# Optimization experiments

Measured on AMD Instinct MI355X. Metric: run time of the kernel, lower is better.

## Reference

```python
import jax, jax.numpy as jnp
import numpy as np

N_SRC, N_DST, N_EDGE, D = 100000, 40000, 600000, 128
LN_EPS = 1e-5

def _mlp(x, w1, b1, w2, b2, g, beta):
    # anemoi MLP: Linear -> SiLU -> Linear -> LayerNorm
    h = jax.nn.silu(x @ w1 + b1)
    h = h @ w2 + b2
    mu = jnp.mean(h, axis=-1, keepdims=True)
    var = jnp.var(h, axis=-1, keepdims=True)
    return (h - mu) * jax.lax.rsqrt(var + LN_EPS) * g + beta

def setup_inputs() -> dict:
    key = jax.random.key(0)
    ks = jax.random.split(key, 12)
    def rn(k, shape, scale):
        return jax.random.normal(k, shape, dtype=jnp.float32) * scale
    w_scale = 0.05
    return dict(
        x_src=rn(ks[0], (N_SRC, D), 1.0),
        x_dst=rn(ks[1], (N_DST, D), 1.0),
        edge_attr=rn(ks[2], (N_EDGE, D), 1.0),
        edge_index=jnp.stack([
            jax.random.randint(ks[3], (N_EDGE,), 0, N_SRC),
            jax.random.randint(ks[4], (N_EDGE,), 0, N_DST)]).astype(jnp.int32),
        edge_w1=rn(ks[5], (3 * D, D), w_scale), edge_b1=jnp.zeros((D,), jnp.float32),
        edge_w2=rn(ks[6], (D, D), w_scale), edge_b2=jnp.zeros((D,), jnp.float32),
        edge_g=jnp.ones((D,), jnp.float32), edge_beta=jnp.zeros((D,), jnp.float32),
        node_w1=rn(ks[7], (2 * D, D), w_scale), node_b1=jnp.zeros((D,), jnp.float32),
        node_w2=rn(ks[8], (D, D), w_scale), node_b2=jnp.zeros((D,), jnp.float32),
        node_g=jnp.ones((D,), jnp.float32), node_beta=jnp.zeros((D,), jnp.float32),
    )

def reference(x_src, x_dst, edge_attr, edge_index,
              edge_w1, edge_b1, edge_w2, edge_b2, edge_g, edge_beta,
              node_w1, node_b1, node_w2, node_b2, node_g, node_beta):
    src, dst = edge_index[0], edge_index[1]
    # GraphConv message: x_i = dst node feats, x_j = src node feats (PyG source_to_target)
    x_i = x_dst[dst]              # [E, D] gather
    x_j = x_src[src]              # [E, D] gather
    edges_new = _mlp(jnp.concatenate([x_i, x_j, edge_attr], axis=-1),
                     edge_w1, edge_b1, edge_w2, edge_b2, edge_g, edge_beta) + edge_attr
    # sum-aggregate messages to dst nodes (chunked sum == single sum)
    agg = jax.ops.segment_sum(edges_new, dst, num_segments=N_DST)  # [N_DST, D]
    nodes_new_dst = _mlp(jnp.concatenate([x_dst, agg], axis=-1),
                         node_w1, node_b1, node_w2, node_b2, node_g, node_beta) + x_dst
    # update_src_nodes=True branch
    nodes_new_src = _mlp(jnp.concatenate([x_src, x_src], axis=-1),
                         node_w1, node_b1, node_w2, node_b2, node_g, node_beta) + x_src
    return nodes_new_src, nodes_new_dst, edges_new
```

## Files before the change

kernel.cpp:

```cpp
#include <hip/hip_runtime.h>
#include <hip/hip_bf16.h>

#define NSRC  100000
#define NDST  40000
#define NEDGE 600000

#define GB_OFF     0ull
#define W1F_OFF    2048ull
#define W2F_OFF    (W1F_OFF + 98304ull)
#define NW1F_OFF   (W2F_OFF + 32768ull)
#define NW2F_OFF   (NW1F_OFF + 65536ull)
#define NW1SF_OFF  (NW2F_OFF + 32768ull)
#define DEG_OFF    (NW1SF_OFF + 32768ull)
#define CSR_OFF    (DEG_OFF + 160000ull)
#define CUR_OFF    (CSR_OFF + 160016ull)
#define CE_OFF     (CUR_OFF + 160000ull)
#define BSUM_OFF   (CE_OFF + 2400000ull)
#define WS_REQUIRED (BSUM_OFF + 1024ull)

typedef __bf16 bf16;
typedef __attribute__((ext_vector_type(8))) __bf16 bf16x8;
typedef __attribute__((ext_vector_type(4))) float f32x4;

__device__ __forceinline__ unsigned short bfbits(float f) {
    return __builtin_bit_cast(unsigned short, (__bf16)f);
}

__device__ __forceinline__ f32x4 mfma16(bf16x8 a, bf16x8 b, f32x4 c) {
    return __builtin_amdgcn_mfma_f32_16x16x32_bf16(a, b, c, 0, 0, 0);
}

__device__ __forceinline__ bf16x8 pack8(float4 a, float4 b) {
    union { uint4 u; bf16x8 v; } o;
    o.u.x = (unsigned)bfbits(a.x) | ((unsigned)bfbits(a.y) << 16);
    o.u.y = (unsigned)bfbits(a.z) | ((unsigned)bfbits(a.w) << 16);
    o.u.z = (unsigned)bfbits(b.x) | ((unsigned)bfbits(b.y) << 16);
    o.u.w = (unsigned)bfbits(b.z) | ((unsigned)bfbits(b.w) << 16);
    return o.v;
}

__device__ __forceinline__ bf16x8 cvt8p(const float* p) {
    return pack8(*(const float4*)p, *(const float4*)(p + 4));
}

__device__ __forceinline__ void cvt8hl_v(float4 a, float4 b, bf16x8& hi, bf16x8& lo) {
    float v[8] = {a.x, a.y, a.z, a.w, b.x, b.y, b.z, b.w};
    union { uint4 u; bf16x8 v; } H, L;
    unsigned hw[8], lw[8];
#pragma unroll
    for (int i = 0; i < 8; ++i) {
        bf16 h = (bf16)v[i];
        hw[i] = (unsigned)__builtin_bit_cast(unsigned short, h);
        lw[i] = (unsigned)bfbits(v[i] - (float)h);
    }
    H.u.x = hw[0] | (hw[1] << 16); H.u.y = hw[2] | (hw[3] << 16);
    H.u.z = hw[4] | (hw[5] << 16); H.u.w = hw[6] | (hw[7] << 16);
    L.u.x = lw[0] | (lw[1] << 16); L.u.y = lw[2] | (lw[3] << 16);
    L.u.z = lw[4] | (lw[5] << 16); L.u.w = lw[6] | (lw[7] << 16);
    hi = H.v; lo = L.v;
}

__global__ __launch_bounds__(256) void prep_kernel(
    const float* __restrict__ w1, const float* __restrict__ w2,
    const float* __restrict__ nw1, const float* __restrict__ nw2,
    bf16* __restrict__ w1f, bf16* __restrict__ w2f,
    bf16* __restrict__ nw1f, bf16* __restrict__ nw2f, bf16* __restrict__ nw1sf) {
    int i = blockIdx.x * 256 + threadIdx.x;
    if (i < 49152) {
        int j = i & 7, lane = (i >> 3) & 63, f = (i >> 9) & 3;
        int rest = i >> 11; int ks = rest % 12, wc = rest / 12;
        int k = ks * 32 + (lane >> 4) * 8 + j;
        int n = wc * 64 + f * 16 + (lane & 15);
        w1f[i] = (bf16)w1[k * 128 + n];
    } else if (i < 65536) {
        int q = i - 49152;
        int j = q & 7, lane = (q >> 3) & 63, f = (q >> 9) & 3;
        int rest = q >> 11; int ks = rest & 3, wc = rest >> 2;
        int k = ks * 32 + (lane >> 4) * 8 + j;
        int n = wc * 64 + f * 16 + (lane & 15);
        w2f[q] = (bf16)w2[k * 128 + n];
    } else if (i < 98304) {
        int q = i - 65536;
        int j = q & 7, lane = (q >> 3) & 63, f = (q >> 9) & 3;
        int rest = q >> 11; int ks = rest & 7, wc = rest >> 3;
        int k = ks * 32 + (lane >> 4) * 8 + j;
        int n = wc * 64 + f * 16 + (lane & 15);
        nw1f[q] = (bf16)nw1[k * 128 + n];
    } else if (i < 114688) {
        int q = i - 98304;
        int j = q & 7, lane = (q >> 3) & 63, f = (q >> 9) & 3;
        int rest = q >> 11; int ks = rest & 3, wc = rest >> 2;
        int k = ks * 32 + (lane >> 4) * 8 + j;
        int n = wc * 64 + f * 16 + (lane & 15);
        nw2f[q] = (bf16)nw2[k * 128 + n];
    } else {
        int q = i - 114688;
        int j = q & 7, lane = (q >> 3) & 63, f = (q >> 9) & 3;
        int rest = q >> 11; int ks = rest & 3, wc = rest >> 2;
        int k = ks * 32 + (lane >> 4) * 8 + j;
        int n = wc * 64 + f * 16 + (lane & 15);
        nw1sf[q] = (bf16)(nw1[k * 128 + n] + nw1[(k + 128) * 128 + n]);
    }
}

__global__ void select_gbeta(const float* __restrict__ a, const float* __restrict__ b,
                             float* __restrict__ g_out, float* __restrict__ beta_out) {
    int t = threadIdx.x;
    bool a_is_g = (a[0] == 1.0f);
    const float* g  = a_is_g ? a : b;
    const float* be = a_is_g ? b : a;
    g_out[t]    = g[t];
    beta_out[t] = be[t];
}

__global__ __launch_bounds__(256) void hist_kernel(const int* __restrict__ eidx,
                                                   int* __restrict__ deg) {
    int e = blockIdx.x * 256 + threadIdx.x;
    if (e < NEDGE) {
        int d = min(max(eidx[NEDGE + e], 0), NDST - 1);
        atomicAdd(&deg[d], 1);
    }
}

__global__ __launch_bounds__(256) void scan1_kernel(const int* __restrict__ deg,
                                                    int* __restrict__ bsum) {
    __shared__ int wsum[4];
    int i = blockIdx.x * 256 + threadIdx.x;
    int v = (i < NDST) ? deg[i] : 0;
#pragma unroll
    for (int m = 1; m < 64; m <<= 1) v += __shfl_xor(v, m, 64);
    if ((threadIdx.x & 63) == 0) wsum[threadIdx.x >> 6] = v;
    __syncthreads();
    if (threadIdx.x == 0) bsum[blockIdx.x] = wsum[0] + wsum[1] + wsum[2] + wsum[3];
}

__global__ __launch_bounds__(256) void scan2_kernel(int* __restrict__ bsum, int nb) {
    __shared__ int buf[256];
    int t = threadIdx.x;
    int v = (t < nb) ? bsum[t] : 0;
    buf[t] = v;
    __syncthreads();
    for (int off = 1; off < 256; off <<= 1) {
        int add = (t >= off) ? buf[t - off] : 0;
        __syncthreads();
        buf[t] += add;
        __syncthreads();
    }
    if (t < nb) bsum[t] = buf[t] - v;
}

__global__ __launch_bounds__(256) void scan3_kernel(const int* __restrict__ deg,
                                                    const int* __restrict__ bsum,
                                                    int* __restrict__ csr,
                                                    int* __restrict__ cur) {
    __shared__ int buf[256];
    int i = blockIdx.x * 256 + threadIdx.x;
    int t = threadIdx.x;
    int v = (i < NDST) ? deg[i] : 0;
    buf[t] = v;
    __syncthreads();
    for (int off = 1; off < 256; off <<= 1) {
        int add = (t >= off) ? buf[t - off] : 0;
        __syncthreads();
        buf[t] += add;
        __syncthreads();
    }
    if (i < NDST) {
        int excl = bsum[blockIdx.x] + buf[t] - v;
        csr[i] = excl;
        cur[i] = excl;
        if (i == NDST - 1) csr[NDST] = NEDGE;
    }
}

__global__ __launch_bounds__(256) void scatter_kernel(const int* __restrict__ eidx,
                                                      int* __restrict__ cur,
                                                      int* __restrict__ ce) {
    int e = blockIdx.x * 256 + threadIdx.x;
    if (e < NEDGE) {
        int d = min(max(eidx[NEDGE + e], 0), NDST - 1);
        int pos = atomicAdd(&cur[d], 1);
        ce[pos] = e;
    }
}

__device__ __forceinline__ void mlp_tail(
    f32x4 (&acc)[2][4], char* sH, float* redS, float* redQ,
    const bf16x8* w2v, const float* b1, const float* b2,
    const float* g, const float* be,
    int wr, int wc, int lr, int lg, int lane,
    float (&outv)[2][4][4])
{
    {
        float b1c[4];
#pragma unroll
        for (int fc = 0; fc < 4; ++fc) b1c[fc] = b1[wc * 64 + fc * 16 + lr];
#pragma unroll
        for (int fr = 0; fr < 2; ++fr)
#pragma unroll
            for (int fc = 0; fc < 4; ++fc)
#pragma unroll
                for (int rg = 0; rg < 4; ++rg) {
                    int row = wr * 32 + fr * 16 + lg * 4 + rg;
                    int col = wc * 64 + fc * 16 + lr;
                    float v = acc[fr][fc][rg] + b1c[fc];
                    v = v / (1.f + __expf(-v));
                    *(bf16*)(sH + ((row * 256 + col * 2) ^ ((row & 7) << 4))) = (bf16)v;
                }
    }
    __syncthreads();

#pragma unroll
    for (int i = 0; i < 2; ++i)
#pragma unroll
        for (int j = 0; j < 4; ++j) acc[i][j] = f32x4{0.f, 0.f, 0.f, 0.f};
#pragma unroll
    for (int ks = 0; ks < 4; ++ks) {
        bf16x8 a[2], b[4];
#pragma unroll
        for (int f = 0; f < 2; ++f) {
            int ra = wr * 32 + f * 16 + lr;
            a[f] = *(const bf16x8*)(sH + ((ra * 256 + ks * 64 + lg * 16) ^ ((ra & 7) << 4)));
        }
#pragma unroll
        for (int fc = 0; fc < 4; ++fc)
            b[fc] = w2v[((wc * 4 + ks) * 4 + fc) * 64 + lane];
#pragma unroll
        for (int i = 0; i < 2; ++i)
#pragma unroll
            for (int j = 0; j < 4; ++j)
                acc[i][j] = mfma16(a[i], b[j], acc[i][j]);
    }

    float b2c[4], gc[4], bc[4];
#pragma unroll
    for (int fc = 0; fc < 4; ++fc) {
        int col = wc * 64 + fc * 16 + lr;
        b2c[fc] = b2[col]; gc[fc] = g[col]; bc[fc] = be[col];
    }
#pragma unroll
    for (int fr = 0; fr < 2; ++fr)
#pragma unroll
        for (int rg = 0; rg < 4; ++rg) {
            float s = 0.f, sq = 0.f;
#pragma unroll
            for (int fc = 0; fc < 4; ++fc) {
                float v = acc[fr][fc][rg] + b2c[fc];
                acc[fr][fc][rg] = v;
                s += v; sq += v * v;
            }
#pragma unroll
            for (int m = 1; m < 16; m <<= 1) {
                s  += __shfl_xor(s, m, 64);
                sq += __shfl_xor(sq, m, 64);
            }
            if (lr == 0) {
                int row = wr * 32 + fr * 16 + lg * 4 + rg;
                redS[row * 2 + wc] = s;
                redQ[row * 2 + wc] = sq;
            }
        }
    __syncthreads();

#pragma unroll
    for (int fr = 0; fr < 2; ++fr)
#pragma unroll
        for (int rg = 0; rg < 4; ++rg) {
            int row = wr * 32 + fr * 16 + lg * 4 + rg;
            float s  = redS[row * 2] + redS[row * 2 + 1];
            float sq = redQ[row * 2] + redQ[row * 2 + 1];
            float mean = s * (1.f / 128.f);
            float var  = fmaxf(sq * (1.f / 128.f) - mean * mean, 0.f);
            float rstd = rsqrtf(var + 1e-5f);
#pragma unroll
            for (int fc = 0; fc < 4; ++fc)
                outv[fr][fc][rg] = (acc[fr][fc][rg] - mean) * rstd * gc[fc] + bc[fc];
        }
}

__global__ __launch_bounds__(256, 3) void edge_mfma(
    const float* __restrict__ xsrc, const float* __restrict__ xdst,
    const float* __restrict__ attr, const int* __restrict__ eidx,
    const bf16* __restrict__ w1f,  const bf16* __restrict__ w2f,
    const float* __restrict__ b1,  const float* __restrict__ b2,
    const float* __restrict__ g,   const float* __restrict__ be,
    float* __restrict__ oute)
{
    __shared__ __align__(16) char sH[32768];
    __shared__ float redS[256], redQ[256];
    __shared__ int sS[128], sD[128];

    const int t = threadIdx.x;
    const long e0 = (long)blockIdx.x * 128;
    if (t < 128) {
        long e = e0 + t; if (e >= NEDGE) e = NEDGE - 1;
        sS[t] = min(max(eidx[e], 0), NSRC - 1);
        sD[t] = min(max(eidx[NEDGE + e], 0), NDST - 1);
    }
    __syncthreads();

    const int lane = t & 63, w = t >> 6;
    const int wr = w >> 1, wc = w & 1;
    const int lr = lane & 15, lg = lane >> 4;

    const float* xi[4]; const float* xj[4]; const float* at[4];
#pragma unroll
    for (int f = 0; f < 4; ++f) {
        int row = wr * 64 + f * 16 + lr;
        long e = e0 + row; if (e >= NEDGE) e = NEDGE - 1;
        xi[f] = xdst + (long)sD[row] * 128;
        xj[f] = xsrc + (long)sS[row] * 128;
        at[f] = attr + e * 128;
    }

    const bf16x8* w1v = (const bf16x8*)w1f;
    const bf16x8* w2v = (const bf16x8*)w2f;

    f32x4 acc[4][4];
#pragma unroll
    for (int i = 0; i < 4; ++i)
#pragma unroll
        for (int j = 0; j < 4; ++j) acc[i][j] = f32x4{0.f, 0.f, 0.f, 0.f};

#pragma unroll
    for (int ks = 0; ks < 12; ++ks) {
        int koff = (ks & 3) * 32 + lg * 8;
        bf16x8 a[4], b[4];
#pragma unroll
        for (int f = 0; f < 4; ++f) {
            const float* p = (ks < 4 ? xi[f] : ks < 8 ? xj[f] : at[f]) + koff;
            a[f] = cvt8p(p);
        }
#pragma unroll
        for (int fc = 0; fc < 4; ++fc)
            b[fc] = w1v[((wc * 12 + ks) * 4 + fc) * 64 + lane];
#pragma unroll
        for (int f = 0; f < 4; ++f)
#pragma unroll
            for (int j = 0; j < 4; ++j)
                acc[f][j] = mfma16(a[f], b[j], acc[f][j]);
    }

    {
        float b1c[4];
#pragma unroll
        for (int fc = 0; fc < 4; ++fc) b1c[fc] = b1[wc * 64 + fc * 16 + lr];
#pragma unroll
        for (int fr = 0; fr < 4; ++fr)
#pragma unroll
            for (int fc = 0; fc < 4; ++fc)
#pragma unroll
                for (int rg = 0; rg < 4; ++rg) {
                    int row = wr * 64 + fr * 16 + lg * 4 + rg;
                    int col = wc * 64 + fc * 16 + lr;
                    float v = acc[fr][fc][rg] + b1c[fc];
                    v = v / (1.f + __expf(-v));
                    *(bf16*)(sH + ((row * 256 + col * 2) ^ ((row & 7) << 4))) = (bf16)v;
                }
    }
    __syncthreads();

#pragma unroll
    for (int i = 0; i < 4; ++i)
#pragma unroll
        for (int j = 0; j < 4; ++j) acc[i][j] = f32x4{0.f, 0.f, 0.f, 0.f};
#pragma unroll
    for (int ks = 0; ks < 4; ++ks) {
        bf16x8 a[4], b[4];
#pragma unroll
        for (int f = 0; f < 4; ++f) {
            int ra = wr * 64 + f * 16 + lr;
            a[f] = *(const bf16x8*)(sH + ((ra * 256 + ks * 64 + lg * 16) ^ ((ra & 7) << 4)));
        }
#pragma unroll
        for (int fc = 0; fc < 4; ++fc)
            b[fc] = w2v[((wc * 4 + ks) * 4 + fc) * 64 + lane];
#pragma unroll
        for (int f = 0; f < 4; ++f)
#pragma unroll
            for (int j = 0; j < 4; ++j)
                acc[f][j] = mfma16(a[f], b[j], acc[f][j]);
    }

    float b2c[4], gc[4], bc[4];
#pragma unroll
    for (int fc = 0; fc < 4; ++fc) {
        int col = wc * 64 + fc * 16 + lr;
        b2c[fc] = b2[col]; gc[fc] = g[col]; bc[fc] = be[col];
    }
#pragma unroll
    for (int fr = 0; fr < 4; ++fr)
#pragma unroll
        for (int rg = 0; rg < 4; ++rg) {
            float s = 0.f, sq = 0.f;
#pragma unroll
            for (int fc = 0; fc < 4; ++fc) {
                float v = acc[fr][fc][rg] + b2c[fc];
                acc[fr][fc][rg] = v;
                s += v; sq += v * v;
            }
#pragma unroll
            for (int m = 1; m < 16; m <<= 1) {
                s  += __shfl_xor(s, m, 64);
                sq += __shfl_xor(sq, m, 64);
            }
            if (lr == 0) {
                int row = wr * 64 + fr * 16 + lg * 4 + rg;
                redS[row * 2 + wc] = s;
                redQ[row * 2 + wc] = sq;
            }
        }
    __syncthreads();

#pragma unroll
    for (int fr = 0; fr < 4; ++fr)
#pragma unroll
        for (int rg = 0; rg < 4; ++rg) {
            int row = wr * 64 + fr * 16 + lg * 4 + rg;
            float s  = redS[row * 2] + redS[row * 2 + 1];
            float sq = redQ[row * 2] + redQ[row * 2 + 1];
            float mean = s * (1.f / 128.f);
            float var  = fmaxf(sq * (1.f / 128.f) - mean * mean, 0.f);
            float rstd = rsqrtf(var + 1e-5f);
            long e = e0 + row;
            if (e < NEDGE) {
#pragma unroll
                for (int fc = 0; fc < 4; ++fc) {
                    int col = wc * 64 + fc * 16 + lr;
                    float v = (acc[fr][fc][rg] - mean) * rstd * gc[fc] + bc[fc];
                    oute[e * 128 + col] = v + attr[e * 128 + col];
                }
            }
        }
}

__global__ __launch_bounds__(256, 4) void node_src_mfma(
    const float* __restrict__ xsrc,
    const bf16* __restrict__ nw1sf, const bf16* __restrict__ nw2f,
    const float* __restrict__ b1, const float* __restrict__ b2,
    const float* __restrict__ g,  const float* __restrict__ be,
    float* __restrict__ outp)
{
    __shared__ __align__(16) char sH[16384];
    __shared__ float redS[128], redQ[128];

    const int t = threadIdx.x;
    const long r0 = (long)blockIdx.x * 64;
    const int lane = t & 63, w = t >> 6;
    const int wr = w >> 1, wc = w & 1;
    const int lr = lane & 15, lg = lane >> 4;

    long gr0 = r0 + wr * 32 + lr;      if (gr0 >= NSRC) gr0 = NSRC - 1;
    long gr1 = r0 + wr * 32 + 16 + lr; if (gr1 >= NSRC) gr1 = NSRC - 1;
    const float* x0 = xsrc + gr0 * 128;
    const float* x1 = xsrc + gr1 * 128;

    const bf16x8* w1v = (const bf16x8*)nw1sf;
    const bf16x8* w2v = (const bf16x8*)nw2f;

    f32x4 acc[2][4];
#pragma unroll
    for (int i = 0; i < 2; ++i)
#pragma unroll
        for (int j = 0; j < 4; ++j) acc[i][j] = f32x4{0.f, 0.f, 0.f, 0.f};

#pragma unroll
    for (int ks = 0; ks < 4; ++ks) {
        int k0 = ks * 32 + lg * 8;
        bf16x8 a0 = cvt8p(x0 + k0);
        bf16x8 a1 = cvt8p(x1 + k0);
        bf16x8 b[4];
#pragma unroll
        for (int fc = 0; fc < 4; ++fc)
            b[fc] = w1v[((wc * 4 + ks) * 4 + fc) * 64 + lane];
#pragma unroll
        for (int j = 0; j < 4; ++j) {
            acc[0][j] = mfma16(a0, b[j], acc[0][j]);
            acc[1][j] = mfma16(a1, b[j], acc[1][j]);
        }
    }

    float outv[2][4][4];
    mlp_tail(acc, sH, redS, redQ, w2v, b1, b2, g, be, wr, wc, lr, lg, lane, outv);

#pragma unroll
    for (int fr = 0; fr < 2; ++fr)
#pragma unroll
        for (int rg = 0; rg < 4; ++rg) {
            int row = wr * 32 + fr * 16 + lg * 4 + rg;
            long gr = r0 + row;
            if (gr < NSRC) {
#pragma unroll
                for (int fc = 0; fc < 4; ++fc) {
                    int col = wc * 64 + fc * 16 + lr;
                    outp[gr * 128 + col] = outv[fr][fc][rg] + xsrc[gr * 128 + col];
                }
            }
        }
}

__global__ __launch_bounds__(256, 3) void node_dst_mfma(
    const float* __restrict__ xdst, const float* __restrict__ oute,
    const int* __restrict__ csr, const int* __restrict__ ce,
    const bf16* __restrict__ nw1f, const bf16* __restrict__ nw2f,
    const float* __restrict__ b1, const float* __restrict__ b2,
    const float* __restrict__ g,  const float* __restrict__ be,
    float* __restrict__ outp)
{
    __shared__ __align__(16) char sAgg[32768];
    __shared__ __align__(16) char sH[16384];
    __shared__ float redS[128], redQ[128];

    const int t = threadIdx.x;
    const long r0 = (long)blockIdx.x * 64;
    const int lane = t & 63, w = t >> 6;
    const int wr = w >> 1, wc = w & 1;
    const int lr = lane & 15, lg = lane >> 4;

    for (int rr = 0; rr < 16; ++rr) {
        int row = w * 16 + rr;
        long gr = r0 + row;
        int s0 = csr[gr], s1 = csr[gr + 1];
        float ax = 0.f, ay = 0.f, az = 0.f, aw2 = 0.f;
        for (int i = s0 + (lane >> 5); i < s1; i += 2) {
            int e = ce[i];
            float4 vv = *(const float4*)(oute + (long)e * 128 + (lane & 31) * 4);
            ax += vv.x; ay += vv.y; az += vv.z; aw2 += vv.w;
        }
        ax  += __shfl_xor(ax, 32);
        ay  += __shfl_xor(ay, 32);
        az  += __shfl_xor(az, 32);
        aw2 += __shfl_xor(aw2, 32);
        if (lane < 32) {
            float4 o; o.x = ax; o.y = ay; o.z = az; o.w = aw2;
            *(float4*)(sAgg + ((row * 512 + (lane & 31) * 16) ^ ((row & 7) << 4))) = o;
        }
    }
    __syncthreads();

    long gr0 = r0 + wr * 32 + lr;
    long gr1 = gr0 + 16;
    const float* x0 = xdst + gr0 * 128;
    const float* x1 = xdst + gr1 * 128;

    const bf16x8* w1v = (const bf16x8*)nw1f;
    const bf16x8* w2v = (const bf16x8*)nw2f;

    f32x4 acc[2][4];
#pragma unroll
    for (int i = 0; i < 2; ++i)
#pragma unroll
        for (int j = 0; j < 4; ++j) acc[i][j] = f32x4{0.f, 0.f, 0.f, 0.f};

#pragma unroll
    for (int ks = 0; ks < 4; ++ks) {
        int k0 = ks * 32 + lg * 8;
        bf16x8 a0 = cvt8p(x0 + k0);
        bf16x8 a1 = cvt8p(x1 + k0);
        bf16x8 b[4];
#pragma unroll
        for (int fc = 0; fc < 4; ++fc)
            b[fc] = w1v[((wc * 8 + ks) * 4 + fc) * 64 + lane];
#pragma unroll
        for (int j = 0; j < 4; ++j) {
            acc[0][j] = mfma16(a0, b[j], acc[0][j]);
            acc[1][j] = mfma16(a1, b[j], acc[1][j]);
        }
    }
    const int rowl0 = wr * 32 + lr, rowl1 = rowl0 + 16;
#pragma unroll
    for (int ks = 0; ks < 4; ++ks) {
        int base0 = rowl0 * 512 + ks * 128 + lg * 32;
        int base1 = rowl1 * 512 + ks * 128 + lg * 32;
        float4 aA = *(const float4*)(sAgg + ((base0)      ^ ((rowl0 & 7) << 4)));
        float4 aB = *(const float4*)(sAgg + ((base0 + 16) ^ ((rowl0 & 7) << 4)));
        float4 bA = *(const float4*)(sAgg + ((base1)      ^ ((rowl1 & 7) << 4)));
        float4 bB = *(const float4*)(sAgg + ((base1 + 16) ^ ((rowl1 & 7) << 4)));
        bf16x8 h0, l0, h1, l1;
        cvt8hl_v(aA, aB, h0, l0);
        cvt8hl_v(bA, bB, h1, l1);
        bf16x8 b[4];
#pragma unroll
        for (int fc = 0; fc < 4; ++fc)
            b[fc] = w1v[((wc * 8 + 4 + ks) * 4 + fc) * 64 + lane];
#pragma unroll
        for (int j = 0; j < 4; ++j) {
            acc[0][j] = mfma16(h0, b[j], acc[0][j]);
            acc[1][j] = mfma16(h1, b[j], acc[1][j]);
            acc[0][j] = mfma16(l0, b[j], acc[0][j]);
            acc[1][j] = mfma16(l1, b[j], acc[1][j]);
        }
    }

    float outv[2][4][4];
    mlp_tail(acc, sH, redS, redQ, w2v, b1, b2, g, be, wr, wc, lr, lg, lane, outv);

#pragma unroll
    for (int fr = 0; fr < 2; ++fr)
#pragma unroll
        for (int rg = 0; rg < 4; ++rg) {
            int row = wr * 32 + fr * 16 + lg * 4 + rg;
            long gr = r0 + row;
#pragma unroll
            for (int fc = 0; fc < 4; ++fc) {
                int col = wc * 64 + fc * 16 + lr;
                outp[gr * 128 + col] = outv[fr][fc][rg] + xdst[gr * 128 + col];
            }
        }
}

extern "C" void kernel_launch(void* const* d_in, const int* in_sizes, int n_in,
                              void* d_out, int out_size, void* d_ws, size_t ws_size,
                              hipStream_t stream) {
    if (ws_size < WS_REQUIRED) return;

    const float* xsrc = nullptr; const float* xdst = nullptr;
    const float* attr = nullptr; const int*   eidx = nullptr;
    const float* ew1  = nullptr; const float* nw1  = nullptr;
    const float* w2s[2] = {nullptr, nullptr}; int n16384 = 0;
    const float* v128[8] = {nullptr}; int n128 = 0;

    for (int i = 0; i < n_in; ++i) {
        switch (in_sizes[i]) {
            case 12800000: xsrc = (const float*)d_in[i]; break;
            case 5120000:  xdst = (const float*)d_in[i]; break;
            case 76800000: attr = (const float*)d_in[i]; break;
            case 1200000:  eidx = (const int*)d_in[i];   break;
            case 49152:    ew1  = (const float*)d_in[i]; break;
            case 32768:    nw1  = (const float*)d_in[i]; break;
            case 16384:    if (n16384 < 2) w2s[n16384++] = (const float*)d_in[i]; break;
            case 128:      if (n128 < 8)   v128[n128++]  = (const float*)d_in[i]; break;
            default: break;
        }
    }
    if (!xsrc || !xdst || !attr || !eidx || !ew1 || !nw1 || n16384 != 2 || n128 != 8)
        return;

    const float* ew2 = w2s[0];
    const float* nw2 = w2s[1];
    const float* eb1 = v128[0]; const float* eb2 = v128[1];
    const float* egA = v128[2]; const float* egB = v128[3];
    const float* nb1 = v128[4]; const float* nb2 = v128[5];
    const float* ngA = v128[6]; const float* ngB = v128[7];

    char* ws = (char*)d_ws;
    float* egv  = (float*)(ws + GB_OFF);
    float* ebv  = egv + 128;
    float* ngv  = ebv + 128;
    float* nbv  = ngv + 128;
    bf16* w1f   = (bf16*)(ws + W1F_OFF);
    bf16* w2f   = (bf16*)(ws + W2F_OFF);
    bf16* nw1f  = (bf16*)(ws + NW1F_OFF);
    bf16* nw2f  = (bf16*)(ws + NW2F_OFF);
    bf16* nw1sf = (bf16*)(ws + NW1SF_OFF);
    int*  deg   = (int*)(ws + DEG_OFF);
    int*  csr   = (int*)(ws + CSR_OFF);
    int*  cur   = (int*)(ws + CUR_OFF);
    int*  ce    = (int*)(ws + CE_OFF);
    int*  bsum  = (int*)(ws + BSUM_OFF);

    float* out      = (float*)d_out;
    float* out_src  = out;
    float* out_dst  = out + (long)NSRC * 128;
    float* out_edge = out + (long)(NSRC + NDST) * 128;

    const int NB = (NDST + 255) / 256;

    hipMemsetAsync(deg, 0, (size_t)NDST * sizeof(int), stream);
    select_gbeta<<<1, 128, 0, stream>>>(egA, egB, egv, ebv);
    select_gbeta<<<1, 128, 0, stream>>>(ngA, ngB, ngv, nbv);
    prep_kernel<<<512, 256, 0, stream>>>(ew1, ew2, nw1, nw2, w1f, w2f, nw1f, nw2f, nw1sf);

    hist_kernel<<<(NEDGE + 255) / 256, 256, 0, stream>>>(eidx, deg);
    scan1_kernel<<<NB, 256, 0, stream>>>(deg, bsum);
    scan2_kernel<<<1, 256, 0, stream>>>(bsum, NB);
    scan3_kernel<<<NB, 256, 0, stream>>>(deg, bsum, csr, cur);
    scatter_kernel<<<(NEDGE + 255) / 256, 256, 0, stream>>>(eidx, cur, ce);

    edge_mfma<<<(NEDGE + 127) / 128, 256, 0, stream>>>(
        xsrc, xdst, attr, eidx, w1f, w2f, eb1, eb2, egv, ebv, out_edge);
    node_src_mfma<<<(NSRC + 63) / 64, 256, 0, stream>>>(
        xsrc, nw1sf, nw2f, nb1, nb2, ngv, nbv, out_src);
    node_dst_mfma<<<NDST / 64, 256, 0, stream>>>(
        xdst, out_edge, csr, ce, nw1f, nw2f, nb1, nb2, ngv, nbv, out_dst);
}
```

Baseline: 657.7 us.

## Fuse segment-sum into edge kernel via dst-sorted edges and bf16 CAS atomics

New measurement: 564.8 us. 14.1% less time.

```diff
diff --git a/kernel.cpp b/kernel.cpp
--- a/kernel.cpp
+++ b/kernel.cpp
@@ -16,7 +16,8 @@
 #define CUR_OFF    (CSR_OFF + 160016ull)
 #define CE_OFF     (CUR_OFF + 160000ull)
 #define BSUM_OFF   (CE_OFF + 2400000ull)
-#define WS_REQUIRED (BSUM_OFF + 1024ull)
+#define AGG_OFF    (BSUM_OFF + 1024ull)
+#define WS_REQUIRED (AGG_OFF + 10240000ull)
 
 typedef __bf16 bf16;
 typedef __attribute__((ext_vector_type(8))) __bf16 bf16x8;
@@ -43,21 +44,16 @@
     return pack8(*(const float4*)p, *(const float4*)(p + 4));
 }
 
-__device__ __forceinline__ void cvt8hl_v(float4 a, float4 b, bf16x8& hi, bf16x8& lo) {
-    float v[8] = {a.x, a.y, a.z, a.w, b.x, b.y, b.z, b.w};
-    union { uint4 u; bf16x8 v; } H, L;
-    unsigned hw[8], lw[8];
-#pragma unroll
-    for (int i = 0; i < 8; ++i) {
-        bf16 h = (bf16)v[i];
-        hw[i] = (unsigned)__builtin_bit_cast(unsigned short, h);
-        lw[i] = (unsigned)bfbits(v[i] - (float)h);
-    }
-    H.u.x = hw[0] | (hw[1] << 16); H.u.y = hw[2] | (hw[3] << 16);
-    H.u.z = hw[4] | (hw[5] << 16); H.u.w = hw[6] | (hw[7] << 16);
-    L.u.x = lw[0] | (lw[1] << 16); L.u.y = lw[2] | (lw[3] << 16);
-    L.u.z = lw[4] | (lw[5] << 16); L.u.w = lw[6] | (lw[7] << 16);
-    hi = H.v; lo = L.v;
+__device__ __forceinline__ void cas_add2(unsigned* p, float a0, float a1) {
+    unsigned old = __hip_atomic_load(p, __ATOMIC_RELAXED, __HIP_MEMORY_SCOPE_AGENT);
+    while (true) {
+        float f0 = __builtin_bit_cast(float, (old & 0xffffu) << 16) + a0;
+        float f1 = __builtin_bit_cast(float, old & 0xffff0000u) + a1;
+        unsigned nv = (unsigned)bfbits(f0) | ((unsigned)bfbits(f1) << 16);
+        unsigned prev = atomicCAS(p, old, nv);
+        if (prev == old) break;
+        old = prev;
+    }
 }
 
 __global__ __launch_bounds__(256) void prep_kernel(
@@ -278,24 +274,31 @@
         }
 }
 
-__global__ __launch_bounds__(256, 3) void edge_mfma(
+__global__ __launch_bounds__(256, 3) void edge_mfma_sorted(
     const float* __restrict__ xsrc, const float* __restrict__ xdst,
     const float* __restrict__ attr, const int* __restrict__ eidx,
+    const int* __restrict__ ce,
     const bf16* __restrict__ w1f,  const bf16* __restrict__ w2f,
     const float* __restrict__ b1,  const float* __restrict__ b2,
     const float* __restrict__ g,   const float* __restrict__ be,
-    float* __restrict__ oute)
+    float* __restrict__ oute, unsigned* __restrict__ aggw)
 {
     __shared__ __align__(16) char sH[32768];
     __shared__ float redS[256], redQ[256];
-    __shared__ int sS[128], sD[128];
+    __shared__ int sE[128], sS[128], sD[128];
 
     const int t = threadIdx.x;
     const long e0 = (long)blockIdx.x * 128;
     if (t < 128) {
-        long e = e0 + t; if (e >= NEDGE) e = NEDGE - 1;
-        sS[t] = min(max(eidx[e], 0), NSRC - 1);
-        sD[t] = min(max(eidx[NEDGE + e], 0), NDST - 1);
+        long pos = e0 + t;
+        if (pos < NEDGE) {
+            int e = ce[pos];
+            sE[t] = e;
+            sS[t] = min(max(eidx[e], 0), NSRC - 1);
+            sD[t] = min(max(eidx[NEDGE + e], 0), NDST - 1);
+        } else {
+            sE[t] = -1; sS[t] = 0; sD[t] = -1;
+        }
     }
     __syncthreads();
 
@@ -307,10 +310,11 @@
 #pragma unroll
     for (int f = 0; f < 4; ++f) {
         int row = wr * 64 + f * 16 + lr;
-        long e = e0 + row; if (e >= NEDGE) e = NEDGE - 1;
-        xi[f] = xdst + (long)sD[row] * 128;
+        long em = max(sE[row], 0);
+        xi[f] = xdst + (long)sD[row] * 128 * (sD[row] >= 0 ? 1 : 0);
+        if (sD[row] < 0) xi[f] = xdst;
         xj[f] = xsrc + (long)sS[row] * 128;
-        at[f] = attr + e * 128;
+        at[f] = attr + em * 128;
     }
 
     const bf16x8* w1v = (const bf16x8*)w1f;
@@ -422,16 +426,36 @@
             float mean = s * (1.f / 128.f);
             float var  = fmaxf(sq * (1.f / 128.f) - mean * mean, 0.f);
             float rstd = rsqrtf(var + 1e-5f);
-            long e = e0 + row;
-            if (e < NEDGE) {
-#pragma unroll
-                for (int fc = 0; fc < 4; ++fc) {
-                    int col = wc * 64 + fc * 16 + lr;
-                    float v = (acc[fr][fc][rg] - mean) * rstd * gc[fc] + bc[fc];
-                    oute[e * 128 + col] = v + attr[e * 128 + col];
-                }
-            }
-        }
+            int e = sE[row];
+            long em = max(e, 0);
+#pragma unroll
+            for (int fc = 0; fc < 4; ++fc) {
+                int col = wc * 64 + fc * 16 + lr;
+                float v = (acc[fr][fc][rg] - mean) * rstd * gc[fc] + bc[fc];
+                v += attr[em * 128 + col];
+                if (e >= 0) oute[(long)e * 128 + col] = v;
+                *(bf16*)(sH + ((row * 256 + col * 2) ^ ((row & 7) << 4))) = (bf16)v;
+            }
+        }
+    __syncthreads();
+
+    {
+        int p = t & 63;
+        int q0 = (t >> 6) * 32;
+        int cur = sD[q0];
+        float s0 = 0.f, s1 = 0.f;
+        for (int r = q0; r < q0 + 32; ++r) {
+            int d = sD[r];
+            if (d != cur) {
+                if (cur >= 0) cas_add2(aggw + (long)cur * 64 + p, s0, s1);
+                cur = d; s0 = 0.f; s1 = 0.f;
+            }
+            unsigned u = *(const unsigned*)(sH + ((r * 256 + p * 4) ^ ((r & 7) << 4)));
+            s0 += __builtin_bit_cast(float, (u & 0xffffu) << 16);
+            s1 += __builtin_bit_cast(float, u & 0xffff0000u);
+        }
+        if (cur >= 0) cas_add2(aggw + (long)cur * 64 + p, s0, s1);
+    }
 }
 
 __global__ __launch_bounds__(256, 4) void node_src_mfma(
@@ -499,15 +523,13 @@
         }
 }
 
-__global__ __launch_bounds__(256, 3) void node_dst_mfma(
-    const float* __restrict__ xdst, const float* __restrict__ oute,
-    const int* __restrict__ csr, const int* __restrict__ ce,
+__global__ __launch_bounds__(256, 4) void node_dst_mfma(
+    const float* __restrict__ xdst, const bf16* __restrict__ agg16,
     const bf16* __restrict__ nw1f, const bf16* __restrict__ nw2f,
     const float* __restrict__ b1, const float* __restrict__ b2,
     const float* __restrict__ g,  const float* __restrict__ be,
     float* __restrict__ outp)
 {
-    __shared__ __align__(16) char sAgg[32768];
     __shared__ __align__(16) char sH[16384];
     __shared__ float redS[128], redQ[128];
 
@@ -517,31 +539,12 @@
     const int wr = w >> 1, wc = w & 1;
     const int lr = lane & 15, lg = lane >> 4;
 
-    for (int rr = 0; rr < 16; ++rr) {
-        int row = w * 16 + rr;
-        long gr = r0 + row;
-        int s0 = csr[gr], s1 = csr[gr + 1];
-        float ax = 0.f, ay = 0.f, az = 0.f, aw2 = 0.f;
-        for (int i = s0 + (lane >> 5); i < s1; i += 2) {
-            int e = ce[i];
-            float4 vv = *(const float4*)(oute + (long)e * 128 + (lane & 31) * 4);
-            ax += vv.x; ay += vv.y; az += vv.z; aw2 += vv.w;
-        }
-        ax  += __shfl_xor(ax, 32);
-        ay  += __shfl_xor(ay, 32);
-        az  += __shfl_xor(az, 32);
-        aw2 += __shfl_xor(aw2, 32);
-        if (lane < 32) {
-            float4 o; o.x = ax; o.y = ay; o.z = az; o.w = aw2;
-            *(float4*)(sAgg + ((row * 512 + (lane & 31) * 16) ^ ((row & 7) << 4))) = o;
-        }
-    }
-    __syncthreads();
-
     long gr0 = r0 + wr * 32 + lr;
     long gr1 = gr0 + 16;
     const float* x0 = xdst + gr0 * 128;
     const float* x1 = xdst + gr1 * 128;
+    const bf16* a0p = agg16 + gr0 * 128;
+    const bf16* a1p = agg16 + gr1 * 128;
 
     const bf16x8* w1v = (const bf16x8*)nw1f;
     const bf16x8* w2v = (const bf16x8*)nw2f;
@@ -567,28 +570,19 @@
             acc[1][j] = mfma16(a1, b[j], acc[1][j]);
         }
     }
-    const int rowl0 = wr * 32 + lr, rowl1 = rowl0 + 16;
 #pragma unroll
     for (int ks = 0; ks < 4; ++ks) {
-        int base0 = rowl0 * 512 + ks * 128 + lg * 32;
-        int base1 = rowl1 * 512 + ks * 128 + lg * 32;
-        float4 aA = *(const float4*)(sAgg + ((base0)      ^ ((rowl0 & 7) << 4)));
-        float4 aB = *(const float4*)(sAgg + ((base0 + 16) ^ ((rowl0 & 7) << 4)));
-        float4 bA = *(const float4*)(sAgg + ((base1)      ^ ((rowl1 & 7) << 4)));
-        float4 bB = *(const float4*)(sAgg + ((base1 + 16) ^ ((rowl1 & 7) << 4)));
-        bf16x8 h0, l0, h1, l1;
-        cvt8hl_v(aA, aB, h0, l0);
-        cvt8hl_v(bA, bB, h1, l1);
+        int k0 = ks * 32 + lg * 8;
+        bf16x8 a0 = *(const bf16x8*)(a0p + k0);
+        bf16x8 a1 = *(const bf16x8*)(a1p + k0);
         bf16x8 b[4];
 #pragma unroll
         for (int fc = 0; fc < 4; ++fc)
             b[fc] = w1v[((wc * 8 + 4 + ks) * 4 + fc) * 64 + lane];
 #pragma unroll
         for (int j = 0; j < 4; ++j) {
-            acc[0][j] = mfma16(h0, b[j], acc[0][j]);
-            acc[1][j] = mfma16(h1, b[j], acc[1][j]);
-            acc[0][j] = mfma16(l0, b[j], acc[0][j]);
-            acc[1][j] = mfma16(l1, b[j], acc[1][j]);
+            acc[0][j] = mfma16(a0, b[j], acc[0][j]);
+            acc[1][j] = mfma16(a1, b[j], acc[1][j]);
         }
     }
 
@@ -658,6 +652,7 @@
     int*  cur   = (int*)(ws + CUR_OFF);
     int*  ce    = (int*)(ws + CE_OFF);
     int*  bsum  = (int*)(ws + BSUM_OFF);
+    bf16* agg16 = (bf16*)(ws + AGG_OFF);
 
     float* out      = (float*)d_out;
     float* out_src  = out;
@@ -667,6 +662,7 @@
     const int NB = (NDST + 255) / 256;
 
     hipMemsetAsync(deg, 0, (size_t)NDST * sizeof(int), stream);
+    hipMemsetAsync(agg16, 0, 10240000ull, stream);
     select_gbeta<<<1, 128, 0, stream>>>(egA, egB, egv, ebv);
     select_gbeta<<<1, 128, 0, stream>>>(ngA, ngB, ngv, nbv);
     prep_kernel<<<512, 256, 0, stream>>>(ew1, ew2, nw1, nw2, w1f, w2f, nw1f, nw2f, nw1sf);
@@ -677,10 +673,11 @@
     scan3_kernel<<<NB, 256, 0, stream>>>(deg, bsum, csr, cur);
     scatter_kernel<<<(NEDGE + 255) / 256, 256, 0, stream>>>(eidx, cur, ce);
 
-    edge_mfma<<<(NEDGE + 127) / 128, 256, 0, stream>>>(
-        xsrc, xdst, attr, eidx, w1f, w2f, eb1, eb2, egv, ebv, out_edge);
+    edge_mfma_sorted<<<(NEDGE + 127) / 128, 256, 0, stream>>>(
+        xsrc, xdst, attr, eidx, ce, w1f, w2f, eb1, eb2, egv, ebv,
+        out_edge, (unsigned*)agg16);
     node_src_mfma<<<(NSRC + 63) / 64, 256, 0, stream>>>(
         xsrc, nw1sf, nw2f, nb1, nb2, ngv, nbv, out_src);
     node_dst_mfma<<<NDST / 64, 256, 0, stream>>>(
-        xdst, out_edge, csr, ce, nw1f, nw2f, nb1, nb2, ngv, nbv, out_dst);
-}
+        xdst, agg16, nw1f, nw2f, nb1, nb2, ngv, nbv, out_dst);
+}
```
